# Optimization experiments

Hardware: AMD Instinct MI355X
Metric: run time of the kernel (lower is better)

Reference implementation:

```python
import jax, jax.numpy as jnp
import numpy as np

F = 16  # ConvLSTM2D filters

def hard_sigmoid(x):
    # Keras (TF2) hard_sigmoid: clip(0.2*x + 0.5, 0, 1) -- ConvLSTM2D default recurrent_activation
    return jnp.clip(0.2 * x + 0.5, 0.0, 1.0)

def convlstm_1x1(x, W, U, b, reverse):
    # x: [B,T,H,W,C]; W: [C,4F]; U: [F,4F]; b: [4F]
    # 1x1 ConvLSTM2D == per-pixel LSTM; gate order in Keras kernel: i, f, c, o
    B, T, H, Wd, C = x.shape
    xs = jnp.moveaxis(x, 1, 0)  # [T,B,H,W,C]
    h0 = jnp.zeros((B, H, Wd, F), x.dtype)
    c0 = jnp.zeros((B, H, Wd, F), x.dtype)
    def step(carry, xt):
        h, c = carry
        z = jnp.einsum('bhwc,cf->bhwf', xt, W) + jnp.einsum('bhwc,cf->bhwf', h, U) + b
        i, f, g, o = jnp.split(z, 4, axis=-1)
        i = hard_sigmoid(i); f = hard_sigmoid(f); o = hard_sigmoid(o)
        c_new = f * c + i * jnp.tanh(g)
        h_new = o * jnp.tanh(c_new)
        return (h_new, c_new), h_new
    # reverse=True: scan runs backward in time, ys aligned to input order,
    # which matches Keras Bidirectional(go_backwards + output re-reversal).
    _, hs = jax.lax.scan(step, (h0, c0), xs, reverse=reverse)
    return jnp.moveaxis(hs, 0, 1)  # [B,T,H,W,F]

def setup_inputs() -> dict:
    key = jax.random.key(0)
    ks = jax.random.split(key, 13)
    B, T, H, Wd, C = 16, 64, 32, 32, 32
    s = 0.1
    inp = {
        'inputs': jax.random.normal(ks[0], (B, T, H, Wd, C), jnp.float32),
        'Wf': jax.random.normal(ks[1], (C, 4 * F), jnp.float32) * s,
        'Uf': jax.random.normal(ks[2], (F, 4 * F), jnp.float32) * s,
        'bf': jnp.zeros((4 * F,), jnp.float32),
        'Wb': jax.random.normal(ks[3], (C, 4 * F), jnp.float32) * s,
        'Ub': jax.random.normal(ks[4], (F, 4 * F), jnp.float32) * s,
        'bb': jnp.zeros((4 * F,), jnp.float32),
        'w1': jax.random.normal(ks[5], (2 * F, 16), jnp.float32) * s,
        'b1': jnp.zeros((16,), jnp.float32),
        'w2': jax.random.normal(ks[6], (16, 16), jnp.float32) * s,
        'b2': jnp.zeros((16,), jnp.float32),
        'w3': jax.random.normal(ks[7], (16, 10), jnp.float32) * s,
        'b3': jnp.zeros((10,), jnp.float32),
    }
    return inp

def reference(inputs, Wf, Uf, bf, Wb, Ub, bb, w1, b1, w2, b2, w3, b3):
    h_fwd = convlstm_1x1(inputs, Wf, Uf, bf, reverse=False)
    h_bwd = convlstm_1x1(inputs, Wb, Ub, bb, reverse=True)
    x = jnp.concatenate([h_fwd, h_bwd], axis=-1)  # [B,T,H,W,2F]
    x = jnp.einsum('...c,cd->...d', x, w1) + b1
    x = jnp.einsum('...c,cd->...d', x, w2) + b2
    x = jnp.einsum('...c,cd->...d', x, w3) + b3
    return x  # [B,T,H,W,10]
```

## Files before the change

### kernel.cpp

```cpp
#include <hip/hip_runtime.h>
#include <hip/hip_bf16.h>
#include <cstdint>
#include <cstddef>

#define TT 64
#define CC 32
#define FF 16
#define HWSZ 1024
#define NPIX 16384

typedef __attribute__((ext_vector_type(8))) short  short8;
typedef __attribute__((ext_vector_type(4))) float  f32x4;

__device__ __forceinline__ float bf2f(unsigned int u16) {
  union { unsigned int u; float f; } c;
  c.u = u16 << 16;
  return c.f;
}
__device__ __forceinline__ unsigned int f2bf(float f) {
  union { float f; unsigned int u; } c;
  c.f = f;
  unsigned int u = c.u;
  return (u + 0x7fffu + ((u >> 16) & 1u)) >> 16;
}
__device__ __forceinline__ unsigned int pkbf(float a, float b) {
  float2 f2; f2.x = a; f2.y = b;
  __hip_bfloat162 h = __float22bfloat162_rn(f2);
  union { __hip_bfloat162 h; unsigned int u; } c; c.h = h;
  return c.u;
}
__device__ __forceinline__ float clamp01(float x) {
  return fminf(fmaxf(x, 0.0f), 1.0f);
}

#define L2E2 2.8853900817779268f
__device__ __forceinline__ float tanh_e2(float e2arg) {
  const float e = __builtin_exp2f(e2arg);
  const float t = __builtin_amdgcn_rcpf(e + 1.0f);
  return fmaf(-2.0f, t, 1.0f);
}

__global__ __launch_bounds__(512) void fold_kernel(
    const float* __restrict__ w1, const float* __restrict__ b1,
    const float* __restrict__ w2, const float* __restrict__ b2,
    const float* __restrict__ w3, const float* __restrict__ b3,
    float* __restrict__ Wc, float* __restrict__ bc)
{
  __shared__ float w23[16 * 10];
  __shared__ float bb2[16];
  const int t = threadIdx.x;

  if (t < 160) {
    const int k = t / 10, j = t % 10;
    float s = 0.0f;
    #pragma unroll
    for (int m = 0; m < 16; ++m) s = fmaf(w2[k * 16 + m], w3[m * 10 + j], s);
    w23[t] = s;
  }
  if (t < 16) {
    float s = b2[t];
    #pragma unroll
    for (int m = 0; m < 16; ++m) s = fmaf(b1[m], w2[m * 16 + t], s);
    bb2[t] = s;
  }
  __syncthreads();
  if (t < 320) {
    const int k = t / 10, j = t % 10;
    float s = 0.0f;
    #pragma unroll
    for (int m = 0; m < 16; ++m) s = fmaf(w1[k * 16 + m], w23[m * 10 + j], s);
    Wc[t] = s;
  }
  if (t < 10) {
    float s = b3[t];
    #pragma unroll
    for (int m = 0; m < 16; ++m) s = fmaf(bb2[m], w3[m * 10 + t], s);
    bc[t] = s;
  }
}

__global__ __launch_bounds__(256) void lstm_kernel(
    const float* __restrict__ x,
    const float* __restrict__ Wf, const float* __restrict__ Uf, const float* __restrict__ bfp,
    const float* __restrict__ Wb, const float* __restrict__ Ub, const float* __restrict__ bbp,
    unsigned short* __restrict__ hf_out, unsigned short* __restrict__ hb_out)
{
  const int dir = blockIdx.y;
  const float* __restrict__ Wp = dir ? Wb : Wf;
  const float* __restrict__ Up = dir ? Ub : Uf;
  const float* __restrict__ bp = dir ? bbp : bfp;
  unsigned short* __restrict__ hout = dir ? hb_out : hf_out;

  const int tid  = threadIdx.x;
  const int lane = tid & 63;
  const int wid  = tid >> 6;
  const int quad = lane >> 4;
  const int l15  = lane & 15;

  const int px  = (blockIdx.x * 4 + wid) * 16 + l15;
  const int b   = px >> 10;
  const int hwi = px & 1023;

  short8 AW[4], AU[4];
  #pragma unroll
  for (int nt = 0; nt < 4; ++nt) {
    short8 vw, vu;
    #pragma unroll
    for (int j = 0; j < 8; ++j) {
      const int k   = quad * 8 + j;
      const int col = nt * 16 + l15;
      vw[j] = (short)f2bf(Wp[k * 64 + col]);
      vu[j] = (k < FF) ? (short)f2bf(Up[k * 64 + col]) : (short)0;
    }
    AW[nt] = vw; AU[nt] = vu;
  }

  float bi[4], bfv[4], bgl[4], bo[4];
  #pragma unroll
  for (int r = 0; r < 4; ++r) {
    const int f = quad * 4 + r;
    bi[r]  = fmaf(bp[ 0 + f], 0.2f, 0.5f);
    bfv[r] = fmaf(bp[16 + f], 0.2f, 0.5f);
    bgl[r] = bp[32 + f] * L2E2;
    bo[r]  = fmaf(bp[48 + f], 0.2f, 0.5f);
  }

  float cst[4] = {0.f, 0.f, 0.f, 0.f};
  union BU { short8 s8; int i[4]; };
  BU Bh; Bh.i[0] = 0; Bh.i[1] = 0; Bh.i[2] = 0; Bh.i[3] = 0;

  const int bp0 = (quad * 32 + l15) * 4;
  const int bp1 = (quad * 32 + 16 + l15) * 4;
  const bool kreal = (quad < 2);

  const int t0 = dir ? (TT - 1) : 0;
  const unsigned int pos0 = (unsigned int)((b * TT + t0) * HWSZ + hwi);
  const int xstep = dir ? -(HWSZ * CC * 4) : (HWSZ * CC * 4);
  const int hstep = dir ? -(HWSZ * 32) : (HWSZ * 32);
  unsigned int hob = pos0 * 32 + quad * 16;

  const char* xb = (const char*)x;
  char* hbb = (char*)hout;

  const unsigned int xo0 = pos0 * (CC * 4) + quad * 32;
  float4 a0 = *reinterpret_cast<const float4*>(xb + xo0);
  float4 a1 = *reinterpret_cast<const float4*>(xb + xo0 + 16);
  const unsigned int xo1 = xo0 + xstep;
  float4 c0 = *reinterpret_cast<const float4*>(xb + xo1);
  float4 c1 = *reinterpret_cast<const float4*>(xb + xo1 + 16);
  unsigned int xoffL = xo1 + xstep;

  f32x4 zx[4];
  {
    BU ax;
    ax.i[0] = pkbf(a0.x, a0.y); ax.i[1] = pkbf(a0.z, a0.w);
    ax.i[2] = pkbf(a1.x, a1.y); ax.i[3] = pkbf(a1.z, a1.w);
    const f32x4 zz = {0.f, 0.f, 0.f, 0.f};
    #pragma unroll
    for (int nt = 0; nt < 4; ++nt)
      zx[nt] = __builtin_amdgcn_mfma_f32_16x16x32_bf16(AW[nt], ax.s8, zz, 0, 0, 0);
  }
  a0 = *reinterpret_cast<const float4*>(xb + xoffL);
  a1 = *reinterpret_cast<const float4*>(xb + xoffL + 16);

  #pragma unroll 2
  for (int s = 0; s < TT; ++s) {
    f32x4 z[4];
    #pragma unroll
    for (int nt = 0; nt < 4; ++nt)
      z[nt] = __builtin_amdgcn_mfma_f32_16x16x32_bf16(AU[nt], Bh.s8, zx[nt], 0, 0, 0);

    {
      const float4 u0 = (s & 1) ? a0 : c0;
      const float4 u1 = (s & 1) ? a1 : c1;
      BU ax;
      ax.i[0] = pkbf(u0.x, u0.y); ax.i[1] = pkbf(u0.z, u0.w);
      ax.i[2] = pkbf(u1.x, u1.y); ax.i[3] = pkbf(u1.z, u1.w);
      const f32x4 zz = {0.f, 0.f, 0.f, 0.f};
      #pragma unroll
      for (int nt = 0; nt < 4; ++nt)
        zx[nt] = __builtin_amdgcn_mfma_f32_16x16x32_bf16(AW[nt], ax.s8, zz, 0, 0, 0);
    }
    if (s + 3 < TT) xoffL += xstep;
    if (s & 1) {
      a0 = *reinterpret_cast<const float4*>(xb + xoffL);
      a1 = *reinterpret_cast<const float4*>(xb + xoffL + 16);
    } else {
      c0 = *reinterpret_cast<const float4*>(xb + xoffL);
      c1 = *reinterpret_cast<const float4*>(xb + xoffL + 16);
    }

    float hv[4];
    #pragma unroll
    for (int r = 0; r < 4; ++r) {
      const float ig = clamp01(fmaf(z[0][r], 0.2f, bi[r]));
      const float fg = clamp01(fmaf(z[1][r], 0.2f, bfv[r]));
      const float og = clamp01(fmaf(z[3][r], 0.2f, bo[r]));
      const float gg = tanh_e2(fmaf(z[2][r], L2E2, bgl[r]));
      cst[r] = fmaf(fg, cst[r], ig * gg);
      hv[r]  = og * tanh_e2(cst[r] * L2E2);
    }

    const int p01 = (int)pkbf(hv[0], hv[1]);
    const int p23 = (int)pkbf(hv[2], hv[3]);
    int d0 = __builtin_amdgcn_ds_bpermute(bp0, p01);
    int d1 = __builtin_amdgcn_ds_bpermute(bp0, p23);
    int d2 = __builtin_amdgcn_ds_bpermute(bp1, p01);
    int d3 = __builtin_amdgcn_ds_bpermute(bp1, p23);
    Bh.i[0] = kreal ? d0 : 0;
    Bh.i[1] = kreal ? d1 : 0;
    Bh.i[2] = kreal ? d2 : 0;
    Bh.i[3] = kreal ? d3 : 0;

    if (lane < 32) {
      *reinterpret_cast<short8*>(hbb + hob) = Bh.s8;
    }
    hob += hstep;
  }
}

__global__ __launch_bounds__(256) void dense_kernel(
    const unsigned short* __restrict__ hf, const unsigned short* __restrict__ hb,
    const float* __restrict__ Wc, const float* __restrict__ bc,
    float* __restrict__ out)
{
  const int tid  = threadIdx.x;
  const int lane = tid & 63;
  const int quad = lane >> 4;
  const int l15  = lane & 15;

  short8 Bhi, Blo;
  #pragma unroll
  for (int j = 0; j < 8; ++j) {
    const int k = quad * 8 + j;
    const float v  = (l15 < 10) ? Wc[k * 10 + l15] : 0.0f;
    const unsigned int hi = f2bf(v);
    const float lo = v - bf2f(hi);
    Bhi[j] = (short)hi;
    Blo[j] = (short)f2bf(lo);
  }
  const float bcv = (l15 < 10) ? bc[l15] : 0.0f;

  const unsigned short* __restrict__ src = (quad & 2) ? hb : hf;
  const unsigned int lsub = (quad & 1) * 8;

  const unsigned int gw = (blockIdx.x * 256 + tid) >> 6;

  #pragma unroll
  for (int i = 0; i < 8; ++i) {
    const unsigned int tile  = gw * 8 + i;
    const unsigned int pos16 = tile * 16 + l15;
    const short8 A = *reinterpret_cast<const short8*>(src + pos16 * 16 + lsub);

    f32x4 acc = {bcv, bcv, bcv, bcv};
    acc = __builtin_amdgcn_mfma_f32_16x16x32_bf16(A, Bhi, acc, 0, 0, 0);
    acc = __builtin_amdgcn_mfma_f32_16x16x32_bf16(A, Blo, acc, 0, 0, 0);

    if (l15 < 10) {
      const unsigned int rowbase = tile * 16 + quad * 4;
      #pragma unroll
      for (int r = 0; r < 4; ++r) {
        out[(size_t)(rowbase + r) * 10 + l15] = acc[r];
      }
    }
  }
}

extern "C" void kernel_launch(void* const* d_in, const int* in_sizes, int n_in,
                              void* d_out, int out_size, void* d_ws, size_t ws_size,
                              hipStream_t stream) {
  const float* x   = (const float*)d_in[0];
  const float* Wf  = (const float*)d_in[1];
  const float* Uf  = (const float*)d_in[2];
  const float* bfp = (const float*)d_in[3];
  const float* Wb  = (const float*)d_in[4];
  const float* Ub  = (const float*)d_in[5];
  const float* bbp = (const float*)d_in[6];
  const float* w1  = (const float*)d_in[7];
  const float* b1  = (const float*)d_in[8];
  const float* w2  = (const float*)d_in[9];
  const float* b2  = (const float*)d_in[10];
  const float* w3  = (const float*)d_in[11];
  const float* b3  = (const float*)d_in[12];

  unsigned short* hfbuf = (unsigned short*)d_ws;
  unsigned short* hbbuf = hfbuf + (size_t)NPIX * TT * FF;
  float* Wc = (float*)(hbbuf + (size_t)NPIX * TT * FF);
  float* bc = Wc + 320;

  fold_kernel<<<1, 512, 0, stream>>>(w1, b1, w2, b2, w3, b3, Wc, bc);

  lstm_kernel<<<dim3(256, 2), 256, 0, stream>>>(x, Wf, Uf, bfp, Wb, Ub, bbp, hfbuf, hbbuf);

  dense_kernel<<<2048, 256, 0, stream>>>(hfbuf, hbbuf, Wc, bc, (float*)d_out);
}
```

Before: 279.8 us.

## Use 16x16x16 MFMA for recurrence to drop cross-lane h permutes

Switches the recurrent matmul from a zero-padded K=32 MFMA to the K=16 bf16 MFMA. With that operand layout, each lane's own packed h values form the B operand directly, so the four ds_bpermute shuffles and the masking are removed. It also deepens the input prefetch to four timesteps with a manually unrolled loop and sets a min-blocks-per-SM occupancy hint. The h output store becomes an 8-byte write from every lane. Risks are register pressure from the extra prefetch buffers under the occupancy bound, and the K=16 instruction's different operand mapping.

```diff
diff --git a/kernel.cpp b/kernel.cpp
--- a/kernel.cpp
+++ b/kernel.cpp
@@ -10,6 +10,7 @@
 #define NPIX 16384
 
 typedef __attribute__((ext_vector_type(8))) short  short8;
+typedef __attribute__((ext_vector_type(4))) short  short4v;
 typedef __attribute__((ext_vector_type(4))) float  f32x4;
 
 __device__ __forceinline__ float bf2f(unsigned int u16) {
@@ -79,7 +80,7 @@
   }
 }
 
-__global__ __launch_bounds__(256) void lstm_kernel(
+__global__ __launch_bounds__(256, 2) void lstm_kernel(
     const float* __restrict__ x,
     const float* __restrict__ Wf, const float* __restrict__ Uf, const float* __restrict__ bfp,
     const float* __restrict__ Wb, const float* __restrict__ Ub, const float* __restrict__ bbp,
@@ -101,18 +102,26 @@
   const int b   = px >> 10;
   const int hwi = px & 1023;
 
-  short8 AW[4], AU[4];
+  short8  AW[4];
+  short4v AU[4];
   #pragma unroll
   for (int nt = 0; nt < 4; ++nt) {
-    short8 vw, vu;
+    short8 vw;
     #pragma unroll
     for (int j = 0; j < 8; ++j) {
       const int k   = quad * 8 + j;
       const int col = nt * 16 + l15;
       vw[j] = (short)f2bf(Wp[k * 64 + col]);
-      vu[j] = (k < FF) ? (short)f2bf(Up[k * 64 + col]) : (short)0;
     }
-    AW[nt] = vw; AU[nt] = vu;
+    AW[nt] = vw;
+    short4v vu;
+    #pragma unroll
+    for (int j = 0; j < 4; ++j) {
+      const int k   = quad * 4 + j;
+      const int col = nt * 16 + l15;
+      vu[j] = (short)f2bf(Up[k * 64 + col]);
+    }
+    AU[nt] = vu;
   }
 
   float bi[4], bfv[4], bgl[4], bo[4];
@@ -126,97 +135,92 @@
   }
 
   float cst[4] = {0.f, 0.f, 0.f, 0.f};
-  union BU { short8 s8; int i[4]; };
-  BU Bh; Bh.i[0] = 0; Bh.i[1] = 0; Bh.i[2] = 0; Bh.i[3] = 0;
-
-  const int bp0 = (quad * 32 + l15) * 4;
-  const int bp1 = (quad * 32 + 16 + l15) * 4;
-  const bool kreal = (quad < 2);
+  union BU  { short8  s8; int i[4]; };
+  union BH  { short4v s4; int i[2]; };
+  BH Bh; Bh.i[0] = 0; Bh.i[1] = 0;
 
   const int t0 = dir ? (TT - 1) : 0;
   const unsigned int pos0 = (unsigned int)((b * TT + t0) * HWSZ + hwi);
   const int xstep = dir ? -(HWSZ * CC * 4) : (HWSZ * CC * 4);
   const int hstep = dir ? -(HWSZ * 32) : (HWSZ * 32);
-  unsigned int hob = pos0 * 32 + quad * 16;
+  unsigned int hob = pos0 * 32 + quad * 8;
 
   const char* xb = (const char*)x;
   char* hbb = (char*)hout;
 
   const unsigned int xo0 = pos0 * (CC * 4) + quad * 32;
-  float4 a0 = *reinterpret_cast<const float4*>(xb + xo0);
-  float4 a1 = *reinterpret_cast<const float4*>(xb + xo0 + 16);
-  const unsigned int xo1 = xo0 + xstep;
-  float4 c0 = *reinterpret_cast<const float4*>(xb + xo1);
-  float4 c1 = *reinterpret_cast<const float4*>(xb + xo1 + 16);
-  unsigned int xoffL = xo1 + xstep;
+  float4 t0a = *reinterpret_cast<const float4*>(xb + xo0);
+  float4 t0b = *reinterpret_cast<const float4*>(xb + xo0 + 16);
+  unsigned int xoff = xo0 + xstep;
+  float4 b1a = *reinterpret_cast<const float4*>(xb + xoff);
+  float4 b1b = *reinterpret_cast<const float4*>(xb + xoff + 16);
+  xoff += xstep;
+  float4 b2a = *reinterpret_cast<const float4*>(xb + xoff);
+  float4 b2b = *reinterpret_cast<const float4*>(xb + xoff + 16);
+  xoff += xstep;
+  float4 b3a = *reinterpret_cast<const float4*>(xb + xoff);
+  float4 b3b = *reinterpret_cast<const float4*>(xb + xoff + 16);
+  xoff += xstep;
+  float4 b0a = *reinterpret_cast<const float4*>(xb + xoff);
+  float4 b0b = *reinterpret_cast<const float4*>(xb + xoff + 16);
 
   f32x4 zx[4];
   {
     BU ax;
-    ax.i[0] = pkbf(a0.x, a0.y); ax.i[1] = pkbf(a0.z, a0.w);
-    ax.i[2] = pkbf(a1.x, a1.y); ax.i[3] = pkbf(a1.z, a1.w);
+    ax.i[0] = pkbf(t0a.x, t0a.y); ax.i[1] = pkbf(t0a.z, t0a.w);
+    ax.i[2] = pkbf(t0b.x, t0b.y); ax.i[3] = pkbf(t0b.z, t0b.w);
     const f32x4 zz = {0.f, 0.f, 0.f, 0.f};
     #pragma unroll
     for (int nt = 0; nt < 4; ++nt)
       zx[nt] = __builtin_amdgcn_mfma_f32_16x16x32_bf16(AW[nt], ax.s8, zz, 0, 0, 0);
   }
-  a0 = *reinterpret_cast<const float4*>(xb + xoffL);
-  a1 = *reinterpret_cast<const float4*>(xb + xoffL + 16);
-
-  #pragma unroll 2
-  for (int s = 0; s < TT; ++s) {
-    f32x4 z[4];
-    #pragma unroll
-    for (int nt = 0; nt < 4; ++nt)
-      z[nt] = __builtin_amdgcn_mfma_f32_16x16x32_bf16(AU[nt], Bh.s8, zx[nt], 0, 0, 0);
-
-    {
-      const float4 u0 = (s & 1) ? a0 : c0;
-      const float4 u1 = (s & 1) ? a1 : c1;
-      BU ax;
-      ax.i[0] = pkbf(u0.x, u0.y); ax.i[1] = pkbf(u0.z, u0.w);
-      ax.i[2] = pkbf(u1.x, u1.y); ax.i[3] = pkbf(u1.z, u1.w);
-      const f32x4 zz = {0.f, 0.f, 0.f, 0.f};
-      #pragma unroll
-      for (int nt = 0; nt < 4; ++nt)
-        zx[nt] = __builtin_amdgcn_mfma_f32_16x16x32_bf16(AW[nt], ax.s8, zz, 0, 0, 0);
-    }
-    if (s + 3 < TT) xoffL += xstep;
-    if (s & 1) {
-      a0 = *reinterpret_cast<const float4*>(xb + xoffL);
-      a1 = *reinterpret_cast<const float4*>(xb + xoffL + 16);
-    } else {
-      c0 = *reinterpret_cast<const float4*>(xb + xoffL);
-      c1 = *reinterpret_cast<const float4*>(xb + xoffL + 16);
-    }
-
-    float hv[4];
-    #pragma unroll
-    for (int r = 0; r < 4; ++r) {
-      const float ig = clamp01(fmaf(z[0][r], 0.2f, bi[r]));
-      const float fg = clamp01(fmaf(z[1][r], 0.2f, bfv[r]));
-      const float og = clamp01(fmaf(z[3][r], 0.2f, bo[r]));
-      const float gg = tanh_e2(fmaf(z[2][r], L2E2, bgl[r]));
-      cst[r] = fmaf(fg, cst[r], ig * gg);
-      hv[r]  = og * tanh_e2(cst[r] * L2E2);
-    }
-
-    const int p01 = (int)pkbf(hv[0], hv[1]);
-    const int p23 = (int)pkbf(hv[2], hv[3]);
-    int d0 = __builtin_amdgcn_ds_bpermute(bp0, p01);
-    int d1 = __builtin_amdgcn_ds_bpermute(bp0, p23);
-    int d2 = __builtin_amdgcn_ds_bpermute(bp1, p01);
-    int d3 = __builtin_amdgcn_ds_bpermute(bp1, p23);
-    Bh.i[0] = kreal ? d0 : 0;
-    Bh.i[1] = kreal ? d1 : 0;
-    Bh.i[2] = kreal ? d2 : 0;
-    Bh.i[3] = kreal ? d3 : 0;
-
-    if (lane < 32) {
-      *reinterpret_cast<short8*>(hbb + hob) = Bh.s8;
-    }
-    hob += hstep;
-  }
+
+#define STEP(S, BA, BB) do {                                                   \
+            \
+    f32x4 z_[4];                                                               \
+    _Pragma("unroll")                                                          \
+    for (int nt = 0; nt < 4; ++nt)                                             \
+      z_[nt] = __builtin_amdgcn_mfma_f32_16x16x16bf16_1k(AU[nt], Bh.s4, zx[nt], 0, 0, 0); \
+                     \
+    {                                                                          \
+      BU ax;                                                                   \
+      ax.i[0] = pkbf(BA.x, BA.y); ax.i[1] = pkbf(BA.z, BA.w);                  \
+      ax.i[2] = pkbf(BB.x, BB.y); ax.i[3] = pkbf(BB.z, BB.w);                  \
+      const f32x4 zzv = {0.f, 0.f, 0.f, 0.f};                                  \
+      _Pragma("unroll")                                                        \
+      for (int nt = 0; nt < 4; ++nt)                                           \
+        zx[nt] = __builtin_amdgcn_mfma_f32_16x16x32_bf16(AW[nt], ax.s8, zzv, 0, 0, 0); \
+    }                                                                          \
+          \
+    if ((S) + 5 < TT) xoff += xstep;                                           \
+    BA = *reinterpret_cast<const float4*>(xb + xoff);                          \
+    BB = *reinterpret_cast<const float4*>(xb + xoff + 16);                     \
+                              \
+    float hv[4];                                                               \
+    _Pragma("unroll")                                                          \
+    for (int r = 0; r < 4; ++r) {                                              \
+      const float ig = clamp01(fmaf(z_[0][r], 0.2f, bi[r]));                   \
+      const float fg = clamp01(fmaf(z_[1][r], 0.2f, bfv[r]));                  \
+      const float og = clamp01(fmaf(z_[3][r], 0.2f, bo[r]));                   \
+      const float gg = tanh_e2(fmaf(z_[2][r], L2E2, bgl[r]));                  \
+      cst[r] = fmaf(fg, cst[r], ig * gg);                                      \
+      hv[r]  = og * tanh_e2(cst[r] * L2E2);                                    \
+    }                                                                          \
+            \
+    Bh.i[0] = (int)pkbf(hv[0], hv[1]);                       \
+    Bh.i[1] = (int)pkbf(hv[2], hv[3]);                     \
+         \
+    *reinterpret_cast<int2*>(hbb + hob) = make_int2(Bh.i[0], Bh.i[1]);         \
+    hob += hstep;                                                              \
+  } while (0)
+
+  for (int sb = 0; sb < TT; sb += 4) {
+    STEP(sb + 0, b1a, b1b);
+    STEP(sb + 1, b2a, b2b);
+    STEP(sb + 2, b3a, b3b);
+    STEP(sb + 3, b0a, b0b);
+  }
+#undef STEP
 }
 
 __global__ __launch_bounds__(256) void dense_kernel(
```

Measured after the change: 270.8 us. 1.03x faster.
